# Kernel tuning notes

Hardware: AMD Instinct MI355X
Metric: run time of the kernel (lower is better)

The kernel has to match this reference:

```python
import jax, jax.numpy as jnp
import numpy as np

B, V = 256, 128256

def setup_inputs() -> dict:
    key = jax.random.key(0)
    k1, k2, k3 = jax.random.split(key, 3)
    logits = jax.random.normal(k1, (B, V), dtype=jnp.float32)
    # temperatures in (0, 1.5], with every 8th request greedy (temp == 0)
    u = jax.random.uniform(k2, (B,), dtype=jnp.float32)
    temperatures = jnp.where(jnp.arange(B) % 8 == 0, 0.0, u * 1.4 + 0.1)
    # uniform noise in [0, 1); transformed to Exp(1) inside reference
    noise = jax.random.uniform(k3, (B, V), dtype=jnp.float32)
    return {"logits": logits, "temperatures": temperatures, "noise": noise}

def reference(logits, temperatures, noise):
    logits = logits.astype(jnp.float32)
    greedy_tokens = jnp.argmax(logits, axis=-1)                      # [B]
    scaled = logits / temperatures[:, None]                           # [B, V]
    probs = jax.nn.softmax(scaled, axis=-1)                           # [B, V]
    # torch.empty_like(probs).exponential_(1)  ==  -log(1 - U),  U ~ Uniform[0,1)
    exp_noise = -jnp.log1p(-noise)                                    # Exp(1) noise
    sample_tokens = jnp.argmax(probs / exp_noise, axis=-1)            # Gumbel-max equiv.
    return jnp.where(temperatures == 0, greedy_tokens, sample_tokens)
```

## Files before the change

### kernel.cpp

```cpp
#include <hip/hip_runtime.h>
#include <math.h>


constexpr int TPB = 1024;
constexpr int CHUNKS = 4;

__device__ __forceinline__ void amax_comb(float v, int i, float& bv, int& bi) {
    if (v > bv || (v == bv && i < bi)) { bv = v; bi = i; }
}

__device__ __forceinline__ float gumbel_key(float l, float u, float c) {
    const float w   = 1.0f - u;
    const float enw = __log2f(w) * -0.693147180559945f;
    float p = 0.16666667f;
    p = fmaf(p, u, 0.2f);
    p = fmaf(p, u, 0.25f);
    p = fmaf(p, u, 0.33333333f);
    p = fmaf(p, u, 0.5f);
    p = fmaf(p, u, 1.0f);
    const float en = (u < 0.125f) ? p * u : enw;
    return fmaf(l, c, -__log2f(en));
}

__global__ __launch_bounds__(TPB, 8) void sampler_phase1(
    const float* __restrict__ logits,
    const float* __restrict__ temps,
    const float* __restrict__ noise,
    float* __restrict__ ws_val,
    int* __restrict__ ws_idx, int V)
{
    const int chunk = blockIdx.x & (CHUNKS - 1);
    const int b     = blockIdx.x / CHUNKS;
    const int V4    = V >> 2;
    const int V4c   = V4 / CHUNKS;
    const int gbase = chunk * V4c;
    const float temp = temps[b];
    const float4* __restrict__ lg4 =
        (const float4*)(logits + (size_t)b * V) + gbase;
    const float4* __restrict__ nz4 =
        (const float4*)(noise + (size_t)b * V) + gbase;
    const int t = threadIdx.x;
    const int last = V4c - 1;

    float bv = -INFINITY;
    int   bi = 0x7fffffff;

    if (temp == 0.0f) {
        float4 A = lg4[min(t, last)];
        float4 Bq = lg4[min(t + TPB, last)];
        for (int j = 0; j * TPB < V4c; ++j) {
            const int f = t + j * TPB;
            const float4 l = A;
            A = Bq;
            Bq = lg4[min(f + 2 * TPB, last)];
            if (f < V4c) {
                const int base = (gbase + f) << 2;
                if (l.x > bv) { bv = l.x; bi = base;     }
                if (l.y > bv) { bv = l.y; bi = base + 1; }
                if (l.z > bv) { bv = l.z; bi = base + 2; }
                if (l.w > bv) { bv = l.w; bi = base + 3; }
            }
        }
    } else {
        const float c = (1.0f / temp) * 1.4426950408889634f;
        float4 La = lg4[min(t, last)],       Ua = nz4[min(t, last)];
        float4 Lb = lg4[min(t + TPB, last)], Ub = nz4[min(t + TPB, last)];
        for (int j = 0; j * TPB < V4c; ++j) {
            const int f = t + j * TPB;
            const float4 l = La, u = Ua;
            La = Lb; Ua = Ub;
            const int fn = min(f + 2 * TPB, last);
            Lb = lg4[fn]; Ub = nz4[fn];
            if (f < V4c) {
                const int base = (gbase + f) << 2;
                const float k0 = gumbel_key(l.x, u.x, c);
                const float k1 = gumbel_key(l.y, u.y, c);
                const float k2 = gumbel_key(l.z, u.z, c);
                const float k3 = gumbel_key(l.w, u.w, c);
                if (k0 > bv) { bv = k0; bi = base;     }
                if (k1 > bv) { bv = k1; bi = base + 1; }
                if (k2 > bv) { bv = k2; bi = base + 2; }
                if (k3 > bv) { bv = k3; bi = base + 3; }
            }
        }
    }

    #pragma unroll
    for (int off = 32; off > 0; off >>= 1) {
        const float ov = __shfl_down(bv, off);
        const int   oi = __shfl_down(bi, off);
        amax_comb(ov, oi, bv, bi);
    }

    __shared__ float s_v[TPB / 64];
    __shared__ int   s_i[TPB / 64];
    const int lane = t & 63;
    const int wave = t >> 6;
    if (lane == 0) { s_v[wave] = bv; s_i[wave] = bi; }
    __syncthreads();
    if (t == 0) {
        #pragma unroll
        for (int w = 1; w < TPB / 64; ++w) amax_comb(s_v[w], s_i[w], bv, bi);
        ws_val[blockIdx.x] = bv;
        ws_idx[blockIdx.x] = bi;
    }
}

__global__ void sampler_phase2(const float* __restrict__ ws_val,
                               const int* __restrict__ ws_idx,
                               int* __restrict__ out, int B)
{
    const int b = blockIdx.x * blockDim.x + threadIdx.x;
    if (b >= B) return;
    float bv = -INFINITY;
    int   bi = 0x7fffffff;
    #pragma unroll
    for (int c = 0; c < CHUNKS; ++c) {
        const float v = ws_val[b * CHUNKS + c];
        const int   i = ws_idx[b * CHUNKS + c];
        if (v > bv || (v == bv && i < bi)) { bv = v; bi = i; }
    }
    out[b] = bi;
}

extern "C" void kernel_launch(void* const* d_in, const int* in_sizes, int n_in,
                              void* d_out, int out_size, void* d_ws, size_t ws_size,
                              hipStream_t stream) {
    const float* logits = (const float*)d_in[0];
    const float* temps  = (const float*)d_in[1];
    const float* noise  = (const float*)d_in[2];
    int* out = (int*)d_out;
    const int B = in_sizes[1];
    const int V = in_sizes[0] / B;

    float* ws_val = (float*)d_ws;
    int*   ws_idx = (int*)d_ws + (size_t)B * CHUNKS;

    sampler_phase1<<<B * CHUNKS, TPB, 0, stream>>>(logits, temps, noise,
                                                   ws_val, ws_idx, V);
    sampler_phase2<<<(B + 255) / 256, 256, 0, stream>>>(ws_val, ws_idx, out, B);
}
```

Before: 274.4 us.

## Hand-pipeline loads with inline asm and deeper prefetch across more, smaller blocks

Moves from 1024-thread blocks with 4 chunks per row to 256-thread blocks with 16 chunks per row. Each thread now handles exactly 8 float4 positions in a fully unrolled loop. Loads are issued with inline global_load_dwordx4 asm and explicit s_waitcnt counters, keeping 4 float4 loads per stream in flight instead of 2. The goal is more memory-level parallelism on a bandwidth-bound scan. In exchange, the kernel hard-codes the iteration count, since V4c/TPB must be at most 8 (true for V=128256). The inline asm also bypasses compiler scheduling.

```diff
diff --git a/kernel.cpp b/kernel.cpp
--- a/kernel.cpp
+++ b/kernel.cpp
@@ -2,8 +2,18 @@
 #include <math.h>
 
 
-constexpr int TPB = 1024;
-constexpr int CHUNKS = 4;
+typedef float f32x4 __attribute__((ext_vector_type(4)));
+
+constexpr int TPB    = 256;
+constexpr int CHUNKS = 16;
+constexpr int NIT    = 8;
+
+#define GLOAD4(dst, ptr) \
+    asm volatile("global_load_dwordx4 %0, %1, off" : "=v"(dst) : "v"(ptr))
+#define VWAIT2(N, x, y) \
+    asm volatile("s_waitcnt vmcnt(%c2)" : "+v"(x), "+v"(y) : "i"(N))
+#define VWAIT1(N, x) \
+    asm volatile("s_waitcnt vmcnt(%c1)" : "+v"(x) : "i"(N))
 
 __device__ __forceinline__ void amax_comb(float v, int i, float& bv, int& bi) {
     if (v > bv || (v == bv && i < bi)) { bv = v; bi = i; }
@@ -22,7 +32,35 @@
     return fmaf(l, c, -__log2f(en));
 }
 
-__global__ __launch_bounds__(TPB, 8) void sampler_phase1(
+__device__ __forceinline__ void consume_s(const f32x4 l, const f32x4 u, int f,
+                                          int gbase, int V4c, float c,
+                                          float& bv, int& bi) {
+    if (f < V4c) {
+        const int base = (gbase + f) << 2;
+        const float k0 = gumbel_key(l.x, u.x, c);
+        const float k1 = gumbel_key(l.y, u.y, c);
+        const float k2 = gumbel_key(l.z, u.z, c);
+        const float k3 = gumbel_key(l.w, u.w, c);
+        if (k0 > bv) { bv = k0; bi = base;     }
+        if (k1 > bv) { bv = k1; bi = base + 1; }
+        if (k2 > bv) { bv = k2; bi = base + 2; }
+        if (k3 > bv) { bv = k3; bi = base + 3; }
+    }
+}
+
+__device__ __forceinline__ void consume_g(const f32x4 l, int f,
+                                          int gbase, int V4c,
+                                          float& bv, int& bi) {
+    if (f < V4c) {
+        const int base = (gbase + f) << 2;
+        if (l.x > bv) { bv = l.x; bi = base;     }
+        if (l.y > bv) { bv = l.y; bi = base + 1; }
+        if (l.z > bv) { bv = l.z; bi = base + 2; }
+        if (l.w > bv) { bv = l.w; bi = base + 3; }
+    }
+}
+
+__global__ __launch_bounds__(TPB) void sampler_phase1(
     const float* __restrict__ logits,
     const float* __restrict__ temps,
     const float* __restrict__ noise,
@@ -34,56 +72,87 @@
     const int V4    = V >> 2;
     const int V4c   = V4 / CHUNKS;
     const int gbase = chunk * V4c;
+    const int last  = V4c - 1;
     const float temp = temps[b];
-    const float4* __restrict__ lg4 =
-        (const float4*)(logits + (size_t)b * V) + gbase;
-    const float4* __restrict__ nz4 =
-        (const float4*)(noise + (size_t)b * V) + gbase;
+    const f32x4* __restrict__ lg4 =
+        (const f32x4*)(logits + (size_t)b * V) + gbase;
+    const f32x4* __restrict__ nz4 =
+        (const f32x4*)(noise + (size_t)b * V) + gbase;
     const int t = threadIdx.x;
-    const int last = V4c - 1;
 
     float bv = -INFINITY;
     int   bi = 0x7fffffff;
 
     if (temp == 0.0f) {
-        float4 A = lg4[min(t, last)];
-        float4 Bq = lg4[min(t + TPB, last)];
-        for (int j = 0; j * TPB < V4c; ++j) {
-            const int f = t + j * TPB;
-            const float4 l = A;
-            A = Bq;
-            Bq = lg4[min(f + 2 * TPB, last)];
-            if (f < V4c) {
-                const int base = (gbase + f) << 2;
-                if (l.x > bv) { bv = l.x; bi = base;     }
-                if (l.y > bv) { bv = l.y; bi = base + 1; }
-                if (l.z > bv) { bv = l.z; bi = base + 2; }
-                if (l.w > bv) { bv = l.w; bi = base + 3; }
-            }
-        }
+        f32x4 G[4];
+        #pragma unroll
+        for (int J = 0; J < 4; ++J) {
+            const int f = min(t + J * TPB, last);
+            GLOAD4(G[J], lg4 + f);
+        }
+        {
+            VWAIT1(3, G[0]); consume_g(G[0], t + 0 * TPB, gbase, V4c, bv, bi);
+            const int f = min(t + 4 * TPB, last); GLOAD4(G[0], lg4 + f);
+        }
+        {
+            VWAIT1(3, G[1]); consume_g(G[1], t + 1 * TPB, gbase, V4c, bv, bi);
+            const int f = min(t + 5 * TPB, last); GLOAD4(G[1], lg4 + f);
+        }
+        {
+            VWAIT1(3, G[2]); consume_g(G[2], t + 2 * TPB, gbase, V4c, bv, bi);
+            const int f = min(t + 6 * TPB, last); GLOAD4(G[2], lg4 + f);
+        }
+        {
+            VWAIT1(3, G[3]); consume_g(G[3], t + 3 * TPB, gbase, V4c, bv, bi);
+            const int f = min(t + 7 * TPB, last); GLOAD4(G[3], lg4 + f);
+        }
+        VWAIT1(3, G[0]); consume_g(G[0], t + 4 * TPB, gbase, V4c, bv, bi);
+        VWAIT1(2, G[1]); consume_g(G[1], t + 5 * TPB, gbase, V4c, bv, bi);
+        VWAIT1(1, G[2]); consume_g(G[2], t + 6 * TPB, gbase, V4c, bv, bi);
+        VWAIT1(0, G[3]); consume_g(G[3], t + 7 * TPB, gbase, V4c, bv, bi);
     } else {
         const float c = (1.0f / temp) * 1.4426950408889634f;
-        float4 La = lg4[min(t, last)],       Ua = nz4[min(t, last)];
-        float4 Lb = lg4[min(t + TPB, last)], Ub = nz4[min(t + TPB, last)];
-        for (int j = 0; j * TPB < V4c; ++j) {
-            const int f = t + j * TPB;
-            const float4 l = La, u = Ua;
-            La = Lb; Ua = Ub;
-            const int fn = min(f + 2 * TPB, last);
-            Lb = lg4[fn]; Ub = nz4[fn];
-            if (f < V4c) {
-                const int base = (gbase + f) << 2;
-                const float k0 = gumbel_key(l.x, u.x, c);
-                const float k1 = gumbel_key(l.y, u.y, c);
-                const float k2 = gumbel_key(l.z, u.z, c);
-                const float k3 = gumbel_key(l.w, u.w, c);
-                if (k0 > bv) { bv = k0; bi = base;     }
-                if (k1 > bv) { bv = k1; bi = base + 1; }
-                if (k2 > bv) { bv = k2; bi = base + 2; }
-                if (k3 > bv) { bv = k3; bi = base + 3; }
-            }
-        }
-    }
+        f32x4 L[4], U[4];
+        #pragma unroll
+        for (int J = 0; J < 4; ++J) {
+            const int f = min(t + J * TPB, last);
+            GLOAD4(L[J], lg4 + f);
+            GLOAD4(U[J], nz4 + f);
+        }
+        {
+            VWAIT2(6, L[0], U[0]);
+            consume_s(L[0], U[0], t + 0 * TPB, gbase, V4c, c, bv, bi);
+            const int f = min(t + 4 * TPB, last);
+            GLOAD4(L[0], lg4 + f); GLOAD4(U[0], nz4 + f);
+        }
+        {
+            VWAIT2(6, L[1], U[1]);
+            consume_s(L[1], U[1], t + 1 * TPB, gbase, V4c, c, bv, bi);
+            const int f = min(t + 5 * TPB, last);
+            GLOAD4(L[1], lg4 + f); GLOAD4(U[1], nz4 + f);
+        }
+        {
+            VWAIT2(6, L[2], U[2]);
+            consume_s(L[2], U[2], t + 2 * TPB, gbase, V4c, c, bv, bi);
+            const int f = min(t + 6 * TPB, last);
+            GLOAD4(L[2], lg4 + f); GLOAD4(U[2], nz4 + f);
+        }
+        {
+            VWAIT2(6, L[3], U[3]);
+            consume_s(L[3], U[3], t + 3 * TPB, gbase, V4c, c, bv, bi);
+            const int f = min(t + 7 * TPB, last);
+            GLOAD4(L[3], lg4 + f); GLOAD4(U[3], nz4 + f);
+        }
+        VWAIT2(6, L[0], U[0]);
+        consume_s(L[0], U[0], t + 4 * TPB, gbase, V4c, c, bv, bi);
+        VWAIT2(4, L[1], U[1]);
+        consume_s(L[1], U[1], t + 5 * TPB, gbase, V4c, c, bv, bi);
+        VWAIT2(2, L[2], U[2]);
+        consume_s(L[2], U[2], t + 6 * TPB, gbase, V4c, c, bv, bi);
+        VWAIT2(0, L[3], U[3]);
+        consume_s(L[3], U[3], t + 7 * TPB, gbase, V4c, c, bv, bi);
+    }
+    static_assert(NIT == 8, "pipeline is hand-unrolled for 8 iterations");
 
     #pragma unroll
     for (int off = 32; off > 0; off >>= 1) {
```

After: 277.6 us. Within noise of the previous version (+1.2%).
